# Optimization experiments

Hardware: AMD Instinct MI355X
Metric: run time of the kernel (lower is better)

## Reference

```python
import jax, jax.numpy as jnp
import numpy as np

N = 50000      # num nodes (genes)
E = 800000     # num edges (TF->Target)
IN = 128       # in_channels
HID = 16       # hidden_channels per head
HEADS = 4
OUT = 32       # out_channels
NEG_SLOPE = 0.2  # PyG GATConv leaky_relu slope
EPS = 1e-16


def setup_inputs() -> dict:
    key = jax.random.key(0)
    ks = jax.random.split(key, 11)
    x = jax.random.normal(ks[0], (N, IN), dtype=jnp.float32)
    edge_index = jax.random.randint(ks[1], (2, E), 0, N, dtype=jnp.int32)
    # layer 1: heads=HEADS, concat=True
    W1 = jax.random.normal(ks[2], (IN, HEADS * HID), dtype=jnp.float32) * (1.0 / np.sqrt(IN))
    a_src1 = jax.random.normal(ks[3], (HEADS, HID), dtype=jnp.float32) * 0.1
    a_dst1 = jax.random.normal(ks[4], (HEADS, HID), dtype=jnp.float32) * 0.1
    b1 = jnp.zeros((HEADS * HID,), dtype=jnp.float32)
    # layer 2: heads=1, concat=False
    W2 = jax.random.normal(ks[5], (HEADS * HID, OUT), dtype=jnp.float32) * (1.0 / np.sqrt(HEADS * HID))
    a_src2 = jax.random.normal(ks[6], (1, OUT), dtype=jnp.float32) * 0.1
    a_dst2 = jax.random.normal(ks[7], (1, OUT), dtype=jnp.float32) * 0.1
    b2 = jnp.zeros((OUT,), dtype=jnp.float32)
    return dict(x=x, edge_index=edge_index, W1=W1, a_src1=a_src1, a_dst1=a_dst1, b1=b1,
                W2=W2, a_src2=a_src2, a_dst2=a_dst2, b2=b2)


def gat_layer(x, edge_index, W, a_src, a_dst, b, concat):
    """PyG GATConv (no self-loops, eval mode): gather -> edge attention -> segment softmax -> scatter."""
    n = x.shape[0]
    heads, ch = a_src.shape
    h = (x @ W).reshape(n, heads, ch)                      # [N, H, C]
    alpha_s = jnp.einsum('nhc,hc->nh', h, a_src)           # [N, H]
    alpha_d = jnp.einsum('nhc,hc->nh', h, a_dst)           # [N, H]
    src, dst = edge_index[0], edge_index[1]
    e = jax.nn.leaky_relu(alpha_s[src] + alpha_d[dst], negative_slope=NEG_SLOPE)  # [E, H]
    # numerically stable softmax over incoming edges of each dst node
    m = jax.ops.segment_max(e, dst, num_segments=n)        # [N, H]
    e = jnp.exp(e - m[dst])
    denom = jax.ops.segment_sum(e, dst, num_segments=n)    # [N, H]
    alpha = e / (denom[dst] + EPS)                         # [E, H]
    msg = h[src] * alpha[:, :, None]                       # [E, H, C]
    out = jax.ops.segment_sum(msg, dst, num_segments=n)    # [N, H, C]
    if concat:
        out = out.reshape(n, heads * ch)
    else:
        out = out.mean(axis=1)
    return out + b


def reference(x, edge_index, W1, a_src1, a_dst1, b1, W2, a_src2, a_dst2, b2):
    h = gat_layer(x, edge_index, W1, a_src1, a_dst1, b1, concat=True)   # [N, HEADS*HID]
    h = jax.nn.elu(h)
    out = gat_layer(h, edge_index, W2, a_src2, a_dst2, b2, concat=False)  # [N, OUT]
    return out
```

## Files before the change

### kernel.cpp

```cpp
#include <hip/hip_runtime.h>
#include <math.h>

#define NN 50000
#define NE 800000
#define INCH 128
#define HID1 16
#define H1 4
#define C1 64
#define C2 32
#define NEG 0.2f
#define EPSF 1e-16f
#define CAP 128
#define BSH 7
#define NBKT 391
#define CAPB 3072
#define EPB 2048
#define NPB1 391
#define GB1 782

static __device__ __forceinline__ float lrelu(float v){ return v > 0.f ? v : NEG * v; }


__global__ __launch_bounds__(256) void k_part1(const int* __restrict__ ei, int* bcnt,
                                               int2* __restrict__ pairs){
    __shared__ int hist[512];
    __shared__ int scn[512];
    __shared__ int spos[512];
    __shared__ int gbase[NBKT];
    __shared__ int2 stg[EPB];
    int t = threadIdx.x;
    hist[t] = 0; hist[t + 256] = 0;
    __syncthreads();

    int e0 = blockIdx.x * EPB;
    int tot = NE - e0; if (tot > EPB) tot = EPB;
    int srcv[8], dstv[8], rnk[8], bkt[8];
    #pragma unroll
    for (int k = 0; k < 8; ++k){
        int idx = k * 256 + t;
        if (idx < tot){
            int e = e0 + idx;
            srcv[k] = ei[e];
            dstv[k] = ei[NE + e];
            bkt[k] = dstv[k] >> BSH;
            rnk[k] = atomicAdd(&hist[bkt[k]], 1);
        } else bkt[k] = -1;
    }
    __syncthreads();

    int* sA = hist; int* sB = scn;
    for (int off = 1; off < 512; off <<= 1){
        int v0 = sA[t]       + ((t       >= off) ? sA[t - off]       : 0);
        int v1 = sA[t + 256] + ((t + 256 >= off) ? sA[t + 256 - off] : 0);
        __syncthreads();
        sB[t] = v0; sB[t + 256] = v1;
        __syncthreads();
        int* tmp = sA; sA = sB; sB = tmp;
    }
    for (int b = t; b < NBKT; b += 256){
        int incl = sA[b];
        int excl = (b > 0) ? sA[b - 1] : 0;
        spos[b] = excl;
        int cnt = incl - excl;
        gbase[b] = (cnt > 0) ? atomicAdd(&bcnt[b], cnt) : 0;
    }
    __syncthreads();

    #pragma unroll
    for (int k = 0; k < 8; ++k)
        if (bkt[k] >= 0){
            int2 pr; pr.x = srcv[k]; pr.y = dstv[k];
            stg[spos[bkt[k]] + rnk[k]] = pr;
        }
    __syncthreads();

    for (int i = t; i < tot; i += 256){
        int2 pr = stg[i];
        int b = pr.y >> BSH;
        pairs[(size_t)b * CAPB + gbase[b] + (i - spos[b])] = pr;
    }
}


__global__ __launch_bounds__(256) void k_build2(
        const int2* __restrict__ pairs, const int* __restrict__ bcnt,
        int* __restrict__ rows, int* __restrict__ deg, int* __restrict__ srcs,
        const float* __restrict__ x, const float* __restrict__ W,
        const float* __restrict__ asrc, const float* __restrict__ adst,
        float* __restrict__ h, float* __restrict__ as1, float* __restrict__ ad1){
    __shared__ __align__(16) char smem[76288];
    int t = threadIdx.x;

    if (blockIdx.x < NBKT){
        int2* stg = (int2*)smem;
        int* hist = (int*)(smem + 24576);
        int* scn  = (int*)(smem + 25088);
        int* cur  = (int*)(smem + 25600);
        int b = blockIdx.x;
        int n0 = b << BSH;
        int cnt = bcnt[b];
        if (t < 128) hist[t] = 0;
        __syncthreads();
        const int2* psrc = pairs + (size_t)b * CAPB;
        for (int i = t; i < cnt; i += 256){
            int2 pr = psrc[i];
            stg[i] = pr;
            atomicAdd(&hist[pr.y - n0], 1);
        }
        __syncthreads();
        int v = (t < 128) ? hist[t] : 0;
        if (t < 128) scn[t] = v;
        __syncthreads();
        for (int off = 1; off < 128; off <<= 1){
            int add = (t < 128 && t >= off) ? scn[t - off] : 0;
            __syncthreads();
            if (t < 128) scn[t] += add;
            __syncthreads();
        }
        if (t < 128){
            int base = b * CAPB + (scn[t] - v);
            cur[t] = base;
            int n = n0 + t;
            if (n < NN){ rows[n] = base; deg[n] = v; }
        }
        __syncthreads();
        for (int i = t; i < cnt; i += 256){
            int2 pr = stg[i];
            int p = atomicAdd(&cur[pr.y - n0], 1);
            srcs[p] = pr.x;
        }
    } else {
        float (*XT)[68] = (float(*)[68])smem;
        float* WS = (float*)(smem + 34816);
        float (*ps)[17] = (float(*)[17])(smem + 67584);
        float (*pd)[17] = (float(*)[17])(smem + 71936);
        int bid = blockIdx.x - NBKT;

        int nodeL = t >> 2;
        int kc = t & 3;
        int g = bid * 64 + nodeL;
        int gc = min(g, NN - 1);
        const float4* xr = (const float4*)(x + (size_t)gc * INCH);
        #pragma unroll
        for (int i = 0; i < 8; ++i){
            int k = kc * 32 + i * 4;
            float4 v = xr[k >> 2];
            XT[k + 0][nodeL] = v.x;
            XT[k + 1][nodeL] = v.y;
            XT[k + 2][nodeL] = v.z;
            XT[k + 3][nodeL] = v.w;
        }
        const float4* W4 = (const float4*)W;
        float4* WS4 = (float4*)WS;
        #pragma unroll
        for (int i = 0; i < 8; ++i) WS4[i * 256 + t] = W4[i * 256 + t];
        __syncthreads();

        int tx = t & 15, ty = t >> 4;
        int c4 = tx * 4, n4 = ty * 4;
        float acc[4][4];
        #pragma unroll
        for (int a = 0; a < 4; ++a)
            #pragma unroll
            for (int b2 = 0; b2 < 4; ++b2) acc[a][b2] = 0.f;

        #pragma unroll 8
        for (int k = 0; k < INCH; ++k){
            float4 xa = *(const float4*)&XT[k][n4];
            float4 wb = *(const float4*)&WS[k * C1 + c4];
            const float xv[4] = {xa.x, xa.y, xa.z, xa.w};
            const float wv[4] = {wb.x, wb.y, wb.z, wb.w};
            #pragma unroll
            for (int a = 0; a < 4; ++a)
                #pragma unroll
                for (int b2 = 0; b2 < 4; ++b2)
                    acc[a][b2] = fmaf(xv[a], wv[b2], acc[a][b2]);
        }

        int hd = tx >> 2;
        #pragma unroll
        for (int a = 0; a < 4; ++a){
            int n = bid * 64 + n4 + a;
            if (n < NN){
                float4 o = {acc[a][0], acc[a][1], acc[a][2], acc[a][3]};
                *(float4*)&h[(size_t)n * C1 + c4] = o;
            }
            float sa = 0.f, da = 0.f;
            #pragma unroll
            for (int b2 = 0; b2 < 4; ++b2){
                sa = fmaf(acc[a][b2], asrc[hd * HID1 + (c4 & 15) + b2], sa);
                da = fmaf(acc[a][b2], adst[hd * HID1 + (c4 & 15) + b2], da);
            }
            ps[n4 + a][tx] = sa;
            pd[n4 + a][tx] = da;
        }
        __syncthreads();
        int nd = t & 63, hh = t >> 6;
        int g2 = bid * 64 + nd;
        if (g2 < NN){
            float sa = ps[nd][hh*4+0] + ps[nd][hh*4+1] + ps[nd][hh*4+2] + ps[nd][hh*4+3];
            float da = pd[nd][hh*4+0] + pd[nd][hh*4+1] + pd[nd][hh*4+2] + pd[nd][hh*4+3];
            as1[g2 * H1 + hh] = sa;
            ad1[g2 * H1 + hh] = da;
        }
    }
}


__global__ __launch_bounds__(256) void k_aggA(
        const int* __restrict__ srcs, const int* __restrict__ rows,
        const int* __restrict__ deg, const float* __restrict__ h1,
        const float* __restrict__ as, const float* __restrict__ ad,
        const float* __restrict__ b1, const float* __restrict__ W2,
        const float* __restrict__ a2s, const float* __restrict__ a2d,
        float* __restrict__ h2, float* __restrict__ as2, float* __restrict__ ad2){
    __shared__ float vbuf[4][H1][132];
    __shared__ int   sbuf[4][CAP];
    __shared__ float hpT[4][68];
    __shared__ float WT[C2][76];
    int t = threadIdx.x;
    {
        const float4* W4 = (const float4*)W2;
        #pragma unroll
        for (int h = 0; h < 2; ++h){
            int tt = t + h * 256;
            float4 v = W4[tt];
            int k = tt >> 3, c0 = (tt & 7) * 4;
            WT[c0 + 0][k] = v.x;
            WT[c0 + 1][k] = v.y;
            WT[c0 + 2][k] = v.z;
            WT[c0 + 3][k] = v.w;
        }
    }
    int w = t >> 6, lane = t & 63;
    int hd1 = lane & 3, eb = lane >> 2;
    int hd3 = lane >> 4;
    int node = blockIdx.x * 4 + w;
    int start = rows[node], dg = deg[node];
    float bv = b1[lane];
    float o;

    if (dg <= CAP){
        float adv = ad[node * H1 + hd1];
        float ssum = 0.f;
        for (int j = eb; j < dg; j += 16){
            int s = srcs[start + j];
            float wv = __expf(lrelu(as[s * H1 + hd1] + adv));
            vbuf[w][hd1][j] = wv;
            if (hd1 == 0) sbuf[w][j] = s;
            ssum += wv;
        }
        ssum += __shfl_xor(ssum, 4);
        ssum += __shfl_xor(ssum, 8);
        ssum += __shfl_xor(ssum, 16);
        ssum += __shfl_xor(ssum, 32);
        float inv = 1.f / (__shfl(ssum, hd3) + EPSF);
        float ac0 = 0.f, ac1 = 0.f, ac2 = 0.f, ac3 = 0.f;
        const float* hL = h1 + lane;
        int j = 0;
        for (; j + 3 < dg; j += 4){
            float4 wv4 = *(const float4*)&vbuf[w][hd3][j];
            int4 s4 = *(const int4*)&sbuf[w][j];
            ac0 = fmaf(hL[(size_t)s4.x * C1], wv4.x, ac0);
            ac1 = fmaf(hL[(size_t)s4.y * C1], wv4.y, ac1);
            ac2 = fmaf(hL[(size_t)s4.z * C1], wv4.z, ac2);
            ac3 = fmaf(hL[(size_t)s4.w * C1], wv4.w, ac3);
        }
        for (; j < dg; ++j)
            ac0 = fmaf(hL[(size_t)sbuf[w][j] * C1], vbuf[w][hd3][j], ac0);
        o = (ac0 + ac1 + ac2 + ac3) * inv + bv;
    } else {
        float adv = ad[node * H1 + hd3];
        float ss = 0.f, ac = 0.f;
        const float* hL = h1 + lane;
        for (int j = 0; j < dg; ++j){
            int s = srcs[start + j];
            float wv = __expf(lrelu(as[s * H1 + hd3] + adv));
            ss += wv;
            ac = fmaf(hL[(size_t)s * C1], wv, ac);
        }
        o = ac / (ss + EPSF) + bv;
    }
    hpT[w][lane] = o > 0.f ? o : expm1f(o);
    __syncthreads();

    int c = lane & 31, k0 = (lane >> 5) * 32;
    float a = 0.f;
    #pragma unroll
    for (int kk = 0; kk < 32; kk += 4){
        float4 hv = *(const float4*)&hpT[w][k0 + kk];
        float4 wv = *(const float4*)&WT[c][k0 + kk];
        a = fmaf(hv.x, wv.x, a);
        a = fmaf(hv.y, wv.y, a);
        a = fmaf(hv.z, wv.z, a);
        a = fmaf(hv.w, wv.w, a);
    }
    a += __shfl_xor(a, 32);
    int gn = blockIdx.x * 4 + w;
    if ((lane >> 5) == 0){
        h2[(size_t)gn * C2 + c] = a;
        float sa = a * a2s[c];
        float da = a * a2d[c];
        #pragma unroll
        for (int off = 16; off >= 1; off >>= 1){
            sa += __shfl_xor(sa, off);
            da += __shfl_xor(da, off);
        }
        if (c == 0){ as2[gn] = sa; ad2[gn] = da; }
    }
}


__global__ __launch_bounds__(256) void k_agg2(
        const int* __restrict__ srcs, const int* __restrict__ rows,
        const int* __restrict__ deg, const float* __restrict__ h2,
        const float* __restrict__ as, const float* __restrict__ ad,
        const float* __restrict__ b2, float* __restrict__ out){
    __shared__ float vbuf[8][CAP];
    __shared__ int   sbuf[8][CAP];
    int sl = threadIdx.x >> 5;
    int lane = threadIdx.x & 31;
    int node = blockIdx.x * 8 + sl;
    int start = rows[node], dg = deg[node];
    float adv = ad[node];

    if (dg <= CAP){
        float ssum = 0.f;
        for (int j = lane; j < dg; j += 32){
            int s = srcs[start + j];
            float wv = __expf(lrelu(as[s] + adv));
            vbuf[sl][j] = wv;
            sbuf[sl][j] = s;
            ssum += wv;
        }
        #pragma unroll
        for (int off = 1; off < 32; off <<= 1) ssum += __shfl_xor(ssum, off);
        float inv = 1.f / (ssum + EPSF);
        float ac0 = 0.f, ac1 = 0.f, ac2 = 0.f, ac3 = 0.f;
        const float* hL = h2 + lane;
        int j = 0;
        for (; j + 3 < dg; j += 4){
            float4 wv4 = *(const float4*)&vbuf[sl][j];
            int4 s4 = *(const int4*)&sbuf[sl][j];
            ac0 = fmaf(hL[(size_t)s4.x * C2], wv4.x, ac0);
            ac1 = fmaf(hL[(size_t)s4.y * C2], wv4.y, ac1);
            ac2 = fmaf(hL[(size_t)s4.z * C2], wv4.z, ac2);
            ac3 = fmaf(hL[(size_t)s4.w * C2], wv4.w, ac3);
        }
        for (; j < dg; ++j)
            ac0 = fmaf(hL[(size_t)sbuf[sl][j] * C2], vbuf[sl][j], ac0);
        out[(size_t)node * C2 + lane] = (ac0 + ac1 + ac2 + ac3) * inv + b2[lane];
    } else {
        float ss = 0.f, ac = 0.f;
        const float* hL = h2 + lane;
        for (int j = 0; j < dg; ++j){
            int s = srcs[start + j];
            float wv = __expf(lrelu(as[s] + adv));
            ss += wv;
            ac = fmaf(hL[(size_t)s * C2], wv, ac);
        }
        out[(size_t)node * C2 + lane] = ac / (ss + EPSF) + b2[lane];
    }
}

extern "C" void kernel_launch(void* const* d_in, const int* in_sizes, int n_in,
                              void* d_out, int out_size, void* d_ws, size_t ws_size,
                              hipStream_t stream) {
    const float* x    = (const float*)d_in[0];
    const int*   ei   = (const int*)  d_in[1];
    const float* W1   = (const float*)d_in[2];
    const float* as1w = (const float*)d_in[3];
    const float* ad1w = (const float*)d_in[4];
    const float* b1   = (const float*)d_in[5];
    const float* W2   = (const float*)d_in[6];
    const float* as2w = (const float*)d_in[7];
    const float* ad2w = (const float*)d_in[8];
    const float* b2   = (const float*)d_in[9];
    float* out = (float*)d_out;

    float* p = (float*)d_ws;
    float* h1   = p; p += (size_t)NN * C1;
    float* as1  = p; p += (size_t)NN * H1;
    float* ad1  = p; p += (size_t)NN * H1;
    float* h2   = p; p += (size_t)NN * C2;
    float* as2  = p; p += NN;
    float* ad2  = p; p += NN;
    int* deg  = (int*)p; p += NN;
    int* rows = (int*)p; p += NN;
    int* bcnt = (int*)p; p += NBKT + 57;
    int* srcs = (int*)p; p += (size_t)NBKT * CAPB;
    int2* pairs = (int2*)p;

    dim3 B(256);
    hipMemsetAsync(bcnt, 0, NBKT * sizeof(int), stream);
    k_part1 <<<NPB1, B, 0, stream>>>(ei, bcnt, pairs);
    k_build2<<<NBKT + GB1, B, 0, stream>>>(pairs, bcnt, rows, deg, srcs,
                                           x, W1, as1w, ad1w, h1, as1, ad1);
    k_aggA  <<<NN / 4, B, 0, stream>>>(srcs, rows, deg, h1, as1, ad1, b1,
                                       W2, as2w, ad2w, h2, as2, ad2);
    k_agg2  <<<NN / 8, B, 0, stream>>>(srcs, rows, deg, h2, as2, ad2, b2, out);
}
```

Measured before the change: 189.1 us.

## Store node features h1/h2 in fp16 and gather half2 pairs per lane

```diff
diff --git a/kernel.cpp b/kernel.cpp
--- a/kernel.cpp
+++ b/kernel.cpp
@@ -1,4 +1,5 @@
 #include <hip/hip_runtime.h>
+#include <hip/hip_fp16.h>
 #include <math.h>
 
 #define NN 50000
@@ -87,7 +88,7 @@
         int* __restrict__ rows, int* __restrict__ deg, int* __restrict__ srcs,
         const float* __restrict__ x, const float* __restrict__ W,
         const float* __restrict__ asrc, const float* __restrict__ adst,
-        float* __restrict__ h, float* __restrict__ as1, float* __restrict__ ad1){
+        __half* __restrict__ h, float* __restrict__ as1, float* __restrict__ ad1){
     __shared__ __align__(16) char smem[76288];
     int t = threadIdx.x;
 
@@ -182,8 +183,10 @@
         for (int a = 0; a < 4; ++a){
             int n = bid * 64 + n4 + a;
             if (n < NN){
-                float4 o = {acc[a][0], acc[a][1], acc[a][2], acc[a][3]};
-                *(float4*)&h[(size_t)n * C1 + c4] = o;
+                union { __half2 q[2]; float2 f; } u;
+                u.q[0] = __floats2half2_rn(acc[a][0], acc[a][1]);
+                u.q[1] = __floats2half2_rn(acc[a][2], acc[a][3]);
+                *(float2*)&h[(size_t)n * C1 + c4] = u.f;
             }
             float sa = 0.f, da = 0.f;
             #pragma unroll
@@ -209,11 +212,11 @@
 
 __global__ __launch_bounds__(256) void k_aggA(
         const int* __restrict__ srcs, const int* __restrict__ rows,
-        const int* __restrict__ deg, const float* __restrict__ h1,
+        const int* __restrict__ deg, const __half* __restrict__ h1,
         const float* __restrict__ as, const float* __restrict__ ad,
         const float* __restrict__ b1, const float* __restrict__ W2,
         const float* __restrict__ a2s, const float* __restrict__ a2d,
-        float* __restrict__ h2, float* __restrict__ as2, float* __restrict__ ad2){
+        __half* __restrict__ h2, float* __restrict__ as2, float* __restrict__ ad2){
     __shared__ float vbuf[4][H1][132];
     __shared__ int   sbuf[4][CAP];
     __shared__ float hpT[4][68];
@@ -222,8 +225,8 @@
     {
         const float4* W4 = (const float4*)W2;
         #pragma unroll
-        for (int h = 0; h < 2; ++h){
-            int tt = t + h * 256;
+        for (int hh = 0; hh < 2; ++hh){
+            int tt = t + hh * 256;
             float4 v = W4[tt];
             int k = tt >> 3, c0 = (tt & 7) * 4;
             WT[c0 + 0][k] = v.x;
@@ -234,11 +237,11 @@
     }
     int w = t >> 6, lane = t & 63;
     int hd1 = lane & 3, eb = lane >> 2;
-    int hd3 = lane >> 4;
+    int eh = lane >> 5, c2 = lane & 31;
+    int hd3 = c2 >> 3;
     int node = blockIdx.x * 4 + w;
     int start = rows[node], dg = deg[node];
-    float bv = b1[lane];
-    float o;
+    const __half2* hh2 = (const __half2*)h1;
 
     if (dg <= CAP){
         float adv = ad[node * H1 + hd1];
@@ -256,32 +259,55 @@
         ssum += __shfl_xor(ssum, 32);
         float inv = 1.f / (__shfl(ssum, hd3) + EPSF);
         float ac0 = 0.f, ac1 = 0.f, ac2 = 0.f, ac3 = 0.f;
-        const float* hL = h1 + lane;
         int j = 0;
         for (; j + 3 < dg; j += 4){
-            float4 wv4 = *(const float4*)&vbuf[w][hd3][j];
-            int4 s4 = *(const int4*)&sbuf[w][j];
-            ac0 = fmaf(hL[(size_t)s4.x * C1], wv4.x, ac0);
-            ac1 = fmaf(hL[(size_t)s4.y * C1], wv4.y, ac1);
-            ac2 = fmaf(hL[(size_t)s4.z * C1], wv4.z, ac2);
-            ac3 = fmaf(hL[(size_t)s4.w * C1], wv4.w, ac3);
-        }
-        for (; j < dg; ++j)
-            ac0 = fmaf(hL[(size_t)sbuf[w][j] * C1], vbuf[w][hd3][j], ac0);
-        o = (ac0 + ac1 + ac2 + ac3) * inv + bv;
+            int sA = sbuf[w][j + eh],        sB = sbuf[w][j + 2 + eh];
+            float wA = vbuf[w][hd3][j + eh], wB = vbuf[w][hd3][j + 2 + eh];
+            float2 gA = __half22float2(hh2[(size_t)sA * 32 + c2]);
+            float2 gB = __half22float2(hh2[(size_t)sB * 32 + c2]);
+            ac0 = fmaf(gA.x, wA, ac0);
+            ac1 = fmaf(gA.y, wA, ac1);
+            ac2 = fmaf(gB.x, wB, ac2);
+            ac3 = fmaf(gB.y, wB, ac3);
+        }
+        if (j + 1 < dg){
+            int sA = sbuf[w][j + eh];
+            float wA = vbuf[w][hd3][j + eh];
+            float2 gA = __half22float2(hh2[(size_t)sA * 32 + c2]);
+            ac0 = fmaf(gA.x, wA, ac0);
+            ac1 = fmaf(gA.y, wA, ac1);
+            j += 2;
+        }
+        if (j < dg && eh == 0){
+            int sA = sbuf[w][j];
+            float wA = vbuf[w][hd3][j];
+            float2 gA = __half22float2(hh2[(size_t)sA * 32 + c2]);
+            ac0 = fmaf(gA.x, wA, ac0);
+            ac1 = fmaf(gA.y, wA, ac1);
+        }
+        ac0 += ac2; ac1 += ac3;
+        ac0 += __shfl_xor(ac0, 32);
+        ac1 += __shfl_xor(ac1, 32);
+        if (eh == 0){
+            float2 bv = *(const float2*)&b1[2 * c2];
+            float o0 = ac0 * inv + bv.x;
+            float o1 = ac1 * inv + bv.y;
+            hpT[w][2 * c2]     = o0 > 0.f ? o0 : expm1f(o0);
+            hpT[w][2 * c2 + 1] = o1 > 0.f ? o1 : expm1f(o1);
+        }
     } else {
-        float adv = ad[node * H1 + hd3];
+        int hdf = lane >> 4;
+        float adv = ad[node * H1 + hdf];
         float ss = 0.f, ac = 0.f;
-        const float* hL = h1 + lane;
         for (int j = 0; j < dg; ++j){
             int s = srcs[start + j];
-            float wv = __expf(lrelu(as[s * H1 + hd3] + adv));
+            float wv = __expf(lrelu(as[s * H1 + hdf] + adv));
             ss += wv;
-            ac = fmaf(hL[(size_t)s * C1], wv, ac);
-        }
-        o = ac / (ss + EPSF) + bv;
-    }
-    hpT[w][lane] = o > 0.f ? o : expm1f(o);
+            ac = fmaf(__half2float(h1[(size_t)s * C1 + lane]), wv, ac);
+        }
+        float o = ac / (ss + EPSF) + b1[lane];
+        hpT[w][lane] = o > 0.f ? o : expm1f(o);
+    }
     __syncthreads();
 
     int c = lane & 31, k0 = (lane >> 5) * 32;
@@ -298,7 +324,7 @@
     a += __shfl_xor(a, 32);
     int gn = blockIdx.x * 4 + w;
     if ((lane >> 5) == 0){
-        h2[(size_t)gn * C2 + c] = a;
+        h2[(size_t)gn * C2 + c] = __float2half(a);
         float sa = a * a2s[c];
         float da = a * a2d[c];
         #pragma unroll
@@ -313,7 +339,7 @@
 
 __global__ __launch_bounds__(256) void k_agg2(
         const int* __restrict__ srcs, const int* __restrict__ rows,
-        const int* __restrict__ deg, const float* __restrict__ h2,
+        const int* __restrict__ deg, const __half* __restrict__ h2,
         const float* __restrict__ as, const float* __restrict__ ad,
         const float* __restrict__ b2, float* __restrict__ out){
     __shared__ float vbuf[8][CAP];
@@ -323,6 +349,8 @@
     int node = blockIdx.x * 8 + sl;
     int start = rows[node], dg = deg[node];
     float adv = ad[node];
+    const __half2* hh2 = (const __half2*)h2;
+    int eh = lane >> 4, c2 = lane & 15;
 
     if (dg <= CAP){
         float ssum = 0.f;
@@ -337,27 +365,47 @@
         for (int off = 1; off < 32; off <<= 1) ssum += __shfl_xor(ssum, off);
         float inv = 1.f / (ssum + EPSF);
         float ac0 = 0.f, ac1 = 0.f, ac2 = 0.f, ac3 = 0.f;
-        const float* hL = h2 + lane;
         int j = 0;
         for (; j + 3 < dg; j += 4){
-            float4 wv4 = *(const float4*)&vbuf[sl][j];
-            int4 s4 = *(const int4*)&sbuf[sl][j];
-            ac0 = fmaf(hL[(size_t)s4.x * C2], wv4.x, ac0);
-            ac1 = fmaf(hL[(size_t)s4.y * C2], wv4.y, ac1);
-            ac2 = fmaf(hL[(size_t)s4.z * C2], wv4.z, ac2);
-            ac3 = fmaf(hL[(size_t)s4.w * C2], wv4.w, ac3);
-        }
-        for (; j < dg; ++j)
-            ac0 = fmaf(hL[(size_t)sbuf[sl][j] * C2], vbuf[sl][j], ac0);
-        out[(size_t)node * C2 + lane] = (ac0 + ac1 + ac2 + ac3) * inv + b2[lane];
+            int sA = sbuf[sl][j + eh],   sB = sbuf[sl][j + 2 + eh];
+            float wA = vbuf[sl][j + eh], wB = vbuf[sl][j + 2 + eh];
+            float2 gA = __half22float2(hh2[(size_t)sA * 16 + c2]);
+            float2 gB = __half22float2(hh2[(size_t)sB * 16 + c2]);
+            ac0 = fmaf(gA.x, wA, ac0);
+            ac1 = fmaf(gA.y, wA, ac1);
+            ac2 = fmaf(gB.x, wB, ac2);
+            ac3 = fmaf(gB.y, wB, ac3);
+        }
+        if (j + 1 < dg){
+            int sA = sbuf[sl][j + eh];
+            float wA = vbuf[sl][j + eh];
+            float2 gA = __half22float2(hh2[(size_t)sA * 16 + c2]);
+            ac0 = fmaf(gA.x, wA, ac0);
+            ac1 = fmaf(gA.y, wA, ac1);
+            j += 2;
+        }
+        if (j < dg && eh == 0){
+            int sA = sbuf[sl][j];
+            float wA = vbuf[sl][j];
+            float2 gA = __half22float2(hh2[(size_t)sA * 16 + c2]);
+            ac0 = fmaf(gA.x, wA, ac0);
+            ac1 = fmaf(gA.y, wA, ac1);
+        }
+        ac0 += ac2; ac1 += ac3;
+        ac0 += __shfl_xor(ac0, 16);
+        ac1 += __shfl_xor(ac1, 16);
+        if (eh == 0){
+            float2 bv = *(const float2*)&b2[2 * c2];
+            float2 o; o.x = ac0 * inv + bv.x; o.y = ac1 * inv + bv.y;
+            *(float2*)&out[(size_t)node * C2 + 2 * c2] = o;
+        }
     } else {
         float ss = 0.f, ac = 0.f;
-        const float* hL = h2 + lane;
         for (int j = 0; j < dg; ++j){
             int s = srcs[start + j];
             float wv = __expf(lrelu(as[s] + adv));
             ss += wv;
-            ac = fmaf(hL[(size_t)s * C2], wv, ac);
+            ac = fmaf(__half2float(h2[(size_t)s * C2 + lane]), wv, ac);
         }
         out[(size_t)node * C2 + lane] = ac / (ss + EPSF) + b2[lane];
     }
@@ -379,10 +427,10 @@
     float* out = (float*)d_out;
 
     float* p = (float*)d_ws;
-    float* h1   = p; p += (size_t)NN * C1;
+    __half* h1 = (__half*)p; p += (size_t)NN * C1 / 2;
+    __half* h2 = (__half*)p; p += (size_t)NN * C2 / 2;
     float* as1  = p; p += (size_t)NN * H1;
     float* ad1  = p; p += (size_t)NN * H1;
-    float* h2   = p; p += (size_t)NN * C2;
     float* as2  = p; p += NN;
     float* ad2  = p; p += NN;
     int* deg  = (int*)p; p += NN;
```

After: 181.8 us. 1.04x faster.
